# Optimization experiments

Measured on AMD Instinct MI355X. Metric: run time of the kernel, lower is better.

## Reference

```python
import jax, jax.numpy as jnp
import numpy as np

N, D_IN, D_HID, D_OUT = 100000, 128, 512, 256
EPS = 1e-5


def _kaiming_uniform(k, shape):
    # torch kaiming_uniform_(a=sqrt(5)) -> bound = sqrt(1/fan_in)
    fan_in = shape[1]
    bound = float(np.sqrt(1.0 / fan_in))
    return jax.random.uniform(k, shape, minval=-bound, maxval=bound, dtype=jnp.float32)


def setup_inputs() -> dict:
    key = jax.random.key(0)
    ks = jax.random.split(key, 10)
    in_set = jax.random.normal(ks[0], (N, D_IN), dtype=jnp.float32)
    matA0 = _kaiming_uniform(ks[1], (D_HID, D_IN))
    matB0 = _kaiming_uniform(ks[2], (D_HID, D_IN))
    matA1 = _kaiming_uniform(ks[3], (D_HID, D_HID))
    matB1 = _kaiming_uniform(ks[4], (D_HID, D_HID))
    matA2 = _kaiming_uniform(ks[5], (D_HID, D_HID))
    matB2 = _kaiming_uniform(ks[6], (D_HID, D_HID))
    ln_gamma = jnp.ones((D_HID,), dtype=jnp.float32)
    ln_beta = jnp.zeros((D_HID,), dtype=jnp.float32)
    out_bound = float(np.sqrt(1.0 / D_HID))
    out_w = jax.random.uniform(ks[7], (D_OUT, D_HID), minval=-out_bound, maxval=out_bound, dtype=jnp.float32)
    out_b = jax.random.uniform(ks[8], (D_OUT,), minval=-out_bound, maxval=out_bound, dtype=jnp.float32)
    return {"in_set": in_set, "matA0": matA0, "matB0": matB0, "matA1": matA1, "matB1": matB1,
            "matA2": matA2, "matB2": matB2, "ln_gamma": ln_gamma, "ln_beta": ln_beta,
            "out_w": out_w, "out_b": out_b}


def _layer(h, A, B, g, b):
    # f(x_i) = relu(LN(A x_i + B (sum_j x_j - x_i)))
    # vectorized: h @ (A-B)^T + total_sum @ B^T  (sum-minus-self identity)
    s = h.sum(axis=0)  # [d]
    h = h @ (A - B).T + s @ B.T  # [N, d_hid]
    mu = h.mean(axis=-1, keepdims=True)
    var = jnp.mean((h - mu) ** 2, axis=-1, keepdims=True)
    h = (h - mu) / jnp.sqrt(var + EPS) * g + b
    return jax.nn.relu(h)


def reference(in_set, matA0, matB0, matA1, matB1, matA2, matB2, ln_gamma, ln_beta, out_w, out_b):
    h = _layer(in_set, matA0, matB0, ln_gamma, ln_beta)
    h = _layer(h, matA1, matB1, ln_gamma, ln_beta)
    h = _layer(h, matA2, matB2, ln_gamma, ln_beta)
    h = h.max(axis=0)  # max-pool over set elements -> [d_hid]
    return h @ out_w.T + out_b  # [d_out]
```

## Files before the change

### kernel.cpp

```cpp
#include <hip/hip_runtime.h>
#include <hip/hip_bf16.h>

#define NPTS 100000
#define NPTS_PAD 100096
#define DHID 512
#define EPSV 1e-5f

typedef __attribute__((ext_vector_type(4))) float f32x4;

#define OFF_INBF   0UL
#define OFF_W0     12812288UL
#define OFF_W1     12877824UL
#define OFF_W2     13139968UL
#define OFF_C0     13402112UL
#define OFF_C1     13404160UL
#define OFF_C2     13406208UL
#define OFF_PARTS  13408256UL
#define OFF_PARTS2 16609280UL
#define OFF_PARTS3 16740352UL
#define OFF_H1     16756736UL
#define OFF_H2     68005888UL

typedef const __attribute__((address_space(1))) unsigned int* gp_t;
typedef __attribute__((address_space(3))) unsigned int* lp_t;

__device__ __forceinline__ void async_copy16(const void* g, void* l) {
    __builtin_amdgcn_global_load_lds((gp_t)g, (lp_t)l, 16, 0, 0);
}

__device__ __forceinline__ unsigned pack4_fp8(float a, float b, float c, float d) {
    unsigned v = (unsigned)__builtin_amdgcn_cvt_pk_fp8_f32(a, b, 0, false);
    v = (unsigned)__builtin_amdgcn_cvt_pk_fp8_f32(c, d, (int)v, true);
    return v;
}

__global__ __launch_bounds__(256) void cvt_pack_kernel(const float* __restrict__ in,
                                                       unsigned char* __restrict__ out) {
    long total = (long)NPTS * 2;
    long stride = (long)gridDim.x * blockDim.x;
    for (long idx = (long)blockIdx.x * blockDim.x + threadIdx.x; idx < total; idx += stride) {
        int kt = (int)(idx / NPTS);
        long r = idx - (long)kt * NPTS;
        const float* src = in + r * 128 + kt * 64;
        unsigned dw[16];
#pragma unroll
        for (int j = 0; j < 16; ++j)
            dw[j] = pack4_fp8(src[4 * j], src[4 * j + 1], src[4 * j + 2], src[4 * j + 3]);
        uint4* dst = (uint4*)(out + ((long)kt * NPTS_PAD + r) * 64);
#pragma unroll
        for (int j = 0; j < 4; ++j)
            dst[j] = make_uint4(dw[4 * j], dw[4 * j + 1], dw[4 * j + 2], dw[4 * j + 3]);
    }
}

__global__ __launch_bounds__(256) void wpack_all_kernel(const float* __restrict__ A0,
                                                        const float* __restrict__ B0,
                                                        const float* __restrict__ A1,
                                                        const float* __restrict__ B1,
                                                        const float* __restrict__ A2,
                                                        const float* __restrict__ B2,
                                                        unsigned long long* __restrict__ W0,
                                                        unsigned long long* __restrict__ W1,
                                                        unsigned long long* __restrict__ W2) {
    int idx = blockIdx.x * 256 + threadIdx.x;
    const float *A, *B; unsigned long long* W; int NK, u;
    if (idx < 8192)       { A = A0; B = B0; W = W0; NK = 2; u = idx; }
    else if (idx < 40960) { A = A1; B = B1; W = W1; NK = 8; u = idx - 8192; }
    else                  { A = A2; B = B2; W = W2; NK = 8; u = idx - 40960; if (u >= 32768) return; }
    int KD = NK * 64;
    int lane = u & 63;
    int rest = u >> 6;
    int s = rest & 1;
    int fn = (rest >> 1) & 7;
    int ks = (rest >> 4) % NK;
    int wv = (rest >> 4) / NK;
    int row = wv * 128 + fn * 16 + (lane & 15);
    int kb = ks * 64 + s * 32 + (lane >> 4) * 8;
    const float* sa = A + (long)row * KD + kb;
    const float* sb = B + (long)row * KD + kb;
    unsigned lo = pack4_fp8(sa[0] - sb[0], sa[1] - sb[1], sa[2] - sb[2], sa[3] - sb[3]);
    unsigned hi = pack4_fp8(sa[4] - sb[4], sa[5] - sb[5], sa[6] - sb[6], sa[7] - sb[7]);
    W[u] = ((unsigned long long)hi << 32) | lo;
}

__global__ __launch_bounds__(256) void colsum_in_kernel(const float* __restrict__ in,
                                                        float* __restrict__ parts) {
    __shared__ float sh[256];
    int t = threadIdx.x, blk = blockIdx.x;
    int c = t & 127, half = t >> 7;
    long rbeg = (long)blk * 196 + half;
    long rend = (long)(blk + 1) * 196; if (rend > NPTS) rend = NPTS;
    float s = 0.f;
    for (long r = rbeg; r < rend; r += 2) s += in[r * 128 + c];
    sh[t] = s;
    __syncthreads();
    if (t < 128) parts[blk * 128 + t] = sh[t] + sh[t + 128];
}

__global__ void part_reduceW_kernel(const float* __restrict__ parts, int nparts, int width,
                                    int op, float* __restrict__ out) {
    int g = blockIdx.x, t = threadIdx.x;
    int chunk = (nparts + gridDim.x - 1) / gridDim.x;
    int b0 = g * chunk, b1 = b0 + chunk; if (b1 > nparts) b1 = nparts;
    float s = 0.f;
    for (int b = b0; b < b1; ++b) {
        float v = parts[(long)b * width + t];
        s = (op == 0) ? (s + v) : fmaxf(s, v);
    }
    out[(long)g * width + t] = s;
}

__global__ __launch_bounds__(64) void gemv_fold_kernel(const float* __restrict__ p3, int dsum,
                                                       const float* __restrict__ Bm,
                                                       const float* __restrict__ bias, int op,
                                                       float* __restrict__ out) {
    int j = blockIdx.x, t = threadIdx.x;
    float acc = 0.f;
    for (int d = t; d < dsum; d += 64) {
        float s = 0.f;
#pragma unroll
        for (int g = 0; g < 8; ++g) {
            float v = p3[(long)g * dsum + d];
            s = (op == 0) ? (s + v) : fmaxf(s, v);
        }
        acc += s * Bm[(long)j * dsum + d];
    }
#pragma unroll
    for (int m = 32; m >= 1; m >>= 1) acc += __shfl_down(acc, m);
    if (t == 0) out[j] = acc + (bias ? bias[j] : 0.0f);
}

template<int KD, bool STORE, int REDOP>
__global__ __launch_bounds__(256, 2)
void layer_kernel(const unsigned char* __restrict__ Xp, const unsigned long long* __restrict__ Wp,
                  const float* __restrict__ cvec, const float* __restrict__ gvec,
                  const float* __restrict__ bvec, unsigned char* __restrict__ Hout,
                  float* __restrict__ red_out) {
    static_assert(KD % 64 == 0, "");
    constexpr int NK = KD / 64;
    __shared__ __align__(128) char smem[NK * 4096];

    const int t = threadIdx.x;
    const int lane = t & 63;
    const int wv = t >> 6;
    const int ln15 = lane & 15;
    const int lg = lane >> 4;
    const long row0 = (long)blockIdx.x * 64;

    f32x4 acc[4][8];
#pragma unroll
    for (int i = 0; i < 4; ++i)
#pragma unroll
        for (int j = 0; j < 8; ++j) acc[i][j] = (f32x4){0.f, 0.f, 0.f, 0.f};

    {
        const int sr = t >> 2;
        const int ss = t & 3;
        const char* Xsrc = (const char*)Xp + (row0 + sr) * 64 + ((ss ^ ((sr >> 1) & 3)) * 16);
#pragma unroll
        for (int kt = 0; kt < NK; ++kt)
            async_copy16(Xsrc + (long)kt * (NPTS_PAD * 64), smem + kt * 4096 + t * 16);
    }
    __syncthreads();

#define RD8X(BASE, r, sub) (*(const long*)((BASE) + (r) * 64 + \
        (((((sub) * 2 + (lg >> 1)) ^ (((r) >> 1) & 3)) * 16) + (lg & 1) * 8)))

    const unsigned long long* Wq = Wp + (long)wv * (NK * 16) * 64 + lane;
#pragma unroll
    for (int ks = 0; ks < NK; ++ks) {
        const char* Xs = smem + ks * 4096;
        long a0[4], a1[4];
#pragma unroll
        for (int fm = 0; fm < 4; ++fm) {
            int r = fm * 16 + ln15;
            a0[fm] = RD8X(Xs, r, 0);
            a1[fm] = RD8X(Xs, r, 1);
        }
#pragma unroll
        for (int fn = 0; fn < 8; ++fn) {
            long w0 = (long)Wq[(ks * 16 + fn * 2 + 0) * 64];
            long w1 = (long)Wq[(ks * 16 + fn * 2 + 1) * 64];
#pragma unroll
            for (int fm = 0; fm < 4; ++fm)
                acc[fm][fn] = __builtin_amdgcn_mfma_f32_16x16x32_fp8_fp8(a0[fm], w0, acc[fm][fn], 0, 0, 0);
#pragma unroll
            for (int fm = 0; fm < 4; ++fm)
                acc[fm][fn] = __builtin_amdgcn_mfma_f32_16x16x32_fp8_fp8(a1[fm], w1, acc[fm][fn], 0, 0, 0);
        }
    }
#undef RD8X
    __syncthreads();

    float* lnred_s = (float*)smem;
    float* lnred_q = (float*)(smem + 1024);
    float* lnmv    = (float*)(smem + 2048);

    const int cbase = wv * 128 + ln15;
    float cv[8], gv[8], bv[8];
#pragma unroll
    for (int fn = 0; fn < 8; ++fn) {
        int col = cbase + fn * 16;
        cv[fn] = cvec[col]; gv[fn] = gvec[col]; bv[fn] = bvec[col];
    }

#pragma unroll
    for (int fm = 0; fm < 4; ++fm)
#pragma unroll
        for (int fn = 0; fn < 8; ++fn) acc[fm][fn] += cv[fn];

    float rs[16], rq[16];
#pragma unroll
    for (int fm = 0; fm < 4; ++fm)
#pragma unroll
        for (int j = 0; j < 4; ++j) {
            float s = 0.f, q = 0.f;
#pragma unroll
            for (int fn = 0; fn < 8; ++fn) {
                float x = acc[fm][fn][j];
                s += x; q += x * x;
            }
            rs[fm * 4 + j] = s; rq[fm * 4 + j] = q;
        }
#pragma unroll
    for (int m = 1; m < 16; m <<= 1)
#pragma unroll
        for (int i = 0; i < 16; ++i) {
            rs[i] += __shfl_xor(rs[i], m);
            rq[i] += __shfl_xor(rq[i], m);
        }
    if (ln15 == 0) {
#pragma unroll
        for (int fm = 0; fm < 4; ++fm)
#pragma unroll
            for (int j = 0; j < 4; ++j) {
                int row = fm * 16 + lg * 4 + j;
                lnred_s[row * 4 + wv] = rs[fm * 4 + j];
                lnred_q[row * 4 + wv] = rq[fm * 4 + j];
            }
    }
    __syncthreads();
    if (t < 64) {
        float s = lnred_s[t * 4] + lnred_s[t * 4 + 1] + lnred_s[t * 4 + 2] + lnred_s[t * 4 + 3];
        float q = lnred_q[t * 4] + lnred_q[t * 4 + 1] + lnred_q[t * 4 + 2] + lnred_q[t * 4 + 3];
        float mu = s * (1.0f / 512.0f);
        float var = q * (1.0f / 512.0f) - mu * mu;
        lnmv[t * 2] = mu;
        lnmv[t * 2 + 1] = rsqrtf(var + EPSV);
    }
    __syncthreads();

#pragma unroll
    for (int fm = 0; fm < 4; ++fm)
#pragma unroll
        for (int j = 0; j < 4; ++j) {
            int rloc = fm * 16 + lg * 4 + j;
            long rglob = row0 + rloc;
            bool ok = rglob < NPTS;
            float mu = lnmv[rloc * 2], rstd = lnmv[rloc * 2 + 1];
#pragma unroll
            for (int fn = 0; fn < 8; ++fn) {
                float y = fmaxf((acc[fm][fn][j] - mu) * rstd * gv[fn] + bv[fn], 0.0f);
                acc[fm][fn][j] = ok ? y : 0.0f;
            }
            if (STORE && ok) {
#pragma unroll
                for (int p = 0; p < 4; ++p) {
                    unsigned u = (unsigned)__builtin_amdgcn_cvt_pk_fp8_f32(
                        acc[fm][2 * p][j], acc[fm][2 * p + 1][j], 0, false);
                    int fnA = 2 * p, fnB = 2 * p + 1;
                    Hout[((long)(wv * 2 + (fnA >> 2)) * NPTS_PAD + rglob) * 64 +
                         (fnA & 3) * 16 + ln15] = (unsigned char)(u & 0xff);
                    Hout[((long)(wv * 2 + (fnB >> 2)) * NPTS_PAD + rglob) * 64 +
                         (fnB & 3) * 16 + ln15] = (unsigned char)((u >> 8) & 0xff);
                }
            }
        }

    float cp[8];
#pragma unroll
    for (int fn = 0; fn < 8; ++fn) {
        float p = 0.f;
#pragma unroll
        for (int fm = 0; fm < 4; ++fm)
#pragma unroll
            for (int j = 0; j < 4; ++j) {
                float v = acc[fm][fn][j];
                p = (REDOP == 0) ? (p + v) : fmaxf(p, v);
            }
        cp[fn] = p;
    }
#pragma unroll
    for (int m = 16; m < 64; m <<= 1)
#pragma unroll
        for (int fn = 0; fn < 8; ++fn) {
            float o = __shfl_xor(cp[fn], m);
            cp[fn] = (REDOP == 0) ? (cp[fn] + o) : fmaxf(cp[fn], o);
        }
    if (lane < 16) {
#pragma unroll
        for (int fn = 0; fn < 8; ++fn)
            red_out[(long)blockIdx.x * 512 + wv * 128 + fn * 16 + lane] = cp[fn];
    }
}

extern "C" void kernel_launch(void* const* d_in, const int* in_sizes, int n_in,
                              void* d_out, int out_size, void* d_ws, size_t ws_size,
                              hipStream_t stream) {
    const float* in_set = (const float*)d_in[0];
    const float* A0 = (const float*)d_in[1];
    const float* B0 = (const float*)d_in[2];
    const float* A1 = (const float*)d_in[3];
    const float* B1 = (const float*)d_in[4];
    const float* A2 = (const float*)d_in[5];
    const float* B2 = (const float*)d_in[6];
    const float* ga = (const float*)d_in[7];
    const float* be = (const float*)d_in[8];
    const float* ow = (const float*)d_in[9];
    const float* ob = (const float*)d_in[10];
    float* outp = (float*)d_out;
    char* ws = (char*)d_ws;

    unsigned char* in_f8 = (unsigned char*)(ws + OFF_INBF);
    unsigned long long* W0p = (unsigned long long*)(ws + OFF_W0);
    unsigned long long* W1p = (unsigned long long*)(ws + OFF_W1);
    unsigned long long* W2p = (unsigned long long*)(ws + OFF_W2);
    float* c0 = (float*)(ws + OFF_C0);
    float* c1 = (float*)(ws + OFF_C1);
    float* c2 = (float*)(ws + OFF_C2);
    float* parts = (float*)(ws + OFF_PARTS);
    float* parts2 = (float*)(ws + OFF_PARTS2);
    float* parts3 = (float*)(ws + OFF_PARTS3);
    unsigned char* h1 = (unsigned char*)(ws + OFF_H1);
    unsigned char* h2 = (unsigned char*)(ws + OFF_H2);

    const int nblk = (NPTS + 63) / 64;

    cvt_pack_kernel<<<1024, 256, 0, stream>>>(in_set, in_f8);
    wpack_all_kernel<<<288, 256, 0, stream>>>(A0, B0, A1, B1, A2, B2, W0p, W1p, W2p);

    colsum_in_kernel<<<512, 256, 0, stream>>>(in_set, parts);
    part_reduceW_kernel<<<64, 128, 0, stream>>>(parts, 512, 128, 0, parts2);
    part_reduceW_kernel<<<8, 128, 0, stream>>>(parts2, 64, 128, 0, parts3);
    gemv_fold_kernel<<<512, 64, 0, stream>>>(parts3, 128, B0, nullptr, 0, c0);

    layer_kernel<128, true, 0><<<nblk, 256, 0, stream>>>(in_f8, W0p, c0, ga, be, h1, parts);
    part_reduceW_kernel<<<64, 512, 0, stream>>>(parts, nblk, 512, 0, parts2);
    part_reduceW_kernel<<<8, 512, 0, stream>>>(parts2, 64, 512, 0, parts3);
    gemv_fold_kernel<<<512, 64, 0, stream>>>(parts3, 512, B1, nullptr, 0, c1);

    layer_kernel<512, true, 0><<<nblk, 256, 0, stream>>>(h1, W1p, c1, ga, be, h2, parts);
    part_reduceW_kernel<<<64, 512, 0, stream>>>(parts, nblk, 512, 0, parts2);
    part_reduceW_kernel<<<8, 512, 0, stream>>>(parts2, 64, 512, 0, parts3);
    gemv_fold_kernel<<<512, 64, 0, stream>>>(parts3, 512, B2, nullptr, 0, c2);

    layer_kernel<512, false, 1><<<nblk, 256, 0, stream>>>(h2, W2p, c2, ga, be, nullptr, parts);
    part_reduceW_kernel<<<64, 512, 0, stream>>>(parts, nblk, 512, 1, parts2);
    part_reduceW_kernel<<<8, 512, 0, stream>>>(parts2, 64, 512, 1, parts3);
    gemv_fold_kernel<<<256, 64, 0, stream>>>(parts3, 512, ow, ob, 1, outp);
}
```

Measured before the change: 278.0 us.

## Use row-major permuted FP8 activation layout with pipelined X staging and packed stores

Switches the FP8 activation buffers from a k-tile-major layout (NPTS_PAD stride per 64-column tile) to a row-major layout with a column permutation within each 64-wide tile. Input and weight packing are permuted to match, so each lane's MFMA output can be written as packed 32-bit words instead of scattered single bytes. The X shared-memory fill becomes a multi-stage async pipeline with per-k-step vmcnt waits and barriers rather than one bulk load before compute. The bounds check on the store is dropped, which relies on the padded buffer absorbing writes for rows past NPTS.

Measured after the change: 297.8 us. 1.07x slower.

```diff
diff --git a/kernel.cpp b/kernel.cpp
--- a/kernel.cpp
+++ b/kernel.cpp
@@ -44,9 +44,9 @@
         const float* src = in + r * 128 + kt * 64;
         unsigned dw[16];
 #pragma unroll
-        for (int j = 0; j < 16; ++j)
-            dw[j] = pack4_fp8(src[4 * j], src[4 * j + 1], src[4 * j + 2], src[4 * j + 3]);
-        uint4* dst = (uint4*)(out + ((long)kt * NPTS_PAD + r) * 64);
+        for (int m = 0; m < 16; ++m)
+            dw[m] = pack4_fp8(src[m], src[16 + m], src[32 + m], src[48 + m]);
+        uint4* dst = (uint4*)(out + r * 128 + kt * 64);
 #pragma unroll
         for (int j = 0; j < 4; ++j)
             dst[j] = make_uint4(dw[4 * j], dw[4 * j + 1], dw[4 * j + 2], dw[4 * j + 3]);
@@ -74,12 +74,15 @@
     int fn = (rest >> 1) & 7;
     int ks = (rest >> 4) % NK;
     int wv = (rest >> 4) / NK;
-    int row = wv * 128 + fn * 16 + (lane & 15);
-    int kb = ks * 64 + s * 32 + (lane >> 4) * 8;
-    const float* sa = A + (long)row * KD + kb;
-    const float* sb = B + (long)row * KD + kb;
-    unsigned lo = pack4_fp8(sa[0] - sb[0], sa[1] - sb[1], sa[2] - sb[2], sa[3] - sb[3]);
-    unsigned hi = pack4_fp8(sa[4] - sb[4], sa[5] - sb[5], sa[6] - sb[6], sa[7] - sb[7]);
+    int ln15 = lane & 15, lg = lane >> 4;
+    int row = wv * 128 + fn * 16 + ln15;
+    int c0 = s * 8 + lg * 2;
+    const float* sa = A + (long)row * KD + ks * 64;
+    const float* sb = B + (long)row * KD + ks * 64;
+    unsigned lo = pack4_fp8(sa[c0] - sb[c0], sa[16 + c0] - sb[16 + c0],
+                            sa[32 + c0] - sb[32 + c0], sa[48 + c0] - sb[48 + c0]);
+    unsigned hi = pack4_fp8(sa[c0 + 1] - sb[c0 + 1], sa[17 + c0] - sb[17 + c0],
+                            sa[33 + c0] - sb[33 + c0], sa[49 + c0] - sb[49 + c0]);
     W[u] = ((unsigned long long)hi << 32) | lo;
 }
 
@@ -153,15 +156,16 @@
 #pragma unroll
         for (int j = 0; j < 8; ++j) acc[i][j] = (f32x4){0.f, 0.f, 0.f, 0.f};
 
-    {
-        const int sr = t >> 2;
-        const int ss = t & 3;
-        const char* Xsrc = (const char*)Xp + (row0 + sr) * 64 + ((ss ^ ((sr >> 1) & 3)) * 16);
-#pragma unroll
-        for (int kt = 0; kt < NK; ++kt)
-            async_copy16(Xsrc + (long)kt * (NPTS_PAD * 64), smem + kt * 4096 + t * 16);
-    }
-    __syncthreads();
+    const int sr = t >> 2;
+    const int ss = t & 3;
+    const char* Xsrc = (const char*)Xp + (row0 + sr) * KD + ((ss ^ ((sr >> 1) & 3)) * 16);
+    auto stage_x = [&](int kt) {
+        async_copy16(Xsrc + kt * 64, smem + kt * 4096 + t * 16);
+    };
+
+    stage_x(0);
+    if (NK > 1) stage_x(1);
+    if (NK > 2) stage_x(2);
 
 #define RD8X(BASE, r, sub) (*(const long*)((BASE) + (r) * 64 + \
         (((((sub) * 2 + (lg >> 1)) ^ (((r) >> 1) & 3)) * 16) + (lg & 1) * 8)))
@@ -169,6 +173,13 @@
     const unsigned long long* Wq = Wp + (long)wv * (NK * 16) * 64 + lane;
 #pragma unroll
     for (int ks = 0; ks < NK; ++ks) {
+        if (ks < NK - 2)       asm volatile("s_waitcnt vmcnt(2)" ::: "memory");
+        else if (ks == NK - 2) asm volatile("s_waitcnt vmcnt(1)" ::: "memory");
+        else                   asm volatile("s_waitcnt vmcnt(0)" ::: "memory");
+        __builtin_amdgcn_s_barrier();
+        __builtin_amdgcn_sched_barrier(0);
+        if (ks + 3 < NK) stage_x(ks + 3);
+
         const char* Xs = smem + ks * 4096;
         long a0[4], a1[4];
 #pragma unroll
@@ -263,17 +274,12 @@
                 float y = fmaxf((acc[fm][fn][j] - mu) * rstd * gv[fn] + bv[fn], 0.0f);
                 acc[fm][fn][j] = ok ? y : 0.0f;
             }
-            if (STORE && ok) {
-#pragma unroll
-                for (int p = 0; p < 4; ++p) {
-                    unsigned u = (unsigned)__builtin_amdgcn_cvt_pk_fp8_f32(
-                        acc[fm][2 * p][j], acc[fm][2 * p + 1][j], 0, false);
-                    int fnA = 2 * p, fnB = 2 * p + 1;
-                    Hout[((long)(wv * 2 + (fnA >> 2)) * NPTS_PAD + rglob) * 64 +
-                         (fnA & 3) * 16 + ln15] = (unsigned char)(u & 0xff);
-                    Hout[((long)(wv * 2 + (fnB >> 2)) * NPTS_PAD + rglob) * 64 +
-                         (fnB & 3) * 16 + ln15] = (unsigned char)((u >> 8) & 0xff);
-                }
+            if (STORE) {
+                unsigned ulo = pack4_fp8(acc[fm][0][j], acc[fm][1][j], acc[fm][2][j], acc[fm][3][j]);
+                unsigned uhi = pack4_fp8(acc[fm][4][j], acc[fm][5][j], acc[fm][6][j], acc[fm][7][j]);
+                char* base = (char*)Hout + rglob * DHID + wv * 128 + ln15 * 4;
+                *(unsigned*)(base) = ulo;
+                *(unsigned*)(base + 64) = uhi;
             }
         }
 
```
